# Performance work log

Measured on AMD Instinct MI355X. Metric: run time of the kernel, lower is better.

The kernel has to match this reference:

```python
import jax, jax.numpy as jnp
import numpy as np


def setup_inputs() -> dict:
    key = jax.random.key(0)
    k1, k2 = jax.random.split(key)
    S_src, S_tgt, B, H = 2048, 2048, 16, 256
    out_e = jax.random.normal(k1, (S_src, B, 2 * H), dtype=jnp.float32)
    out_d = jax.random.normal(k2, (S_tgt, B, H), dtype=jnp.float32)
    return {"out_e": out_e, "out_d": out_d}


def reference(out_e, out_d):
    # out_e: [S_src, B, 2*H] (bidirectional), out_d: [S_tgt, B, H]
    S, B, H2 = out_e.shape
    # sum the two directions: [S, B, H]
    enc = out_e.reshape(S, B, 2, H2 // 2).sum(axis=2)
    enc = enc.transpose(1, 0, 2)   # [B, S_src, H]
    dec = out_d.transpose(1, 0, 2)  # [B, S_tgt, H]
    # attn scores [B, S_src, S_tgt]; softmax over source positions (dim=1)
    attn = jnp.einsum('bsh,bth->bst', enc, dec)
    attn = jax.nn.softmax(attn, axis=1)
    # context: weighted sum over source positions -> [B, S_tgt, H]
    context = jnp.einsum('bst,bsh->bth', attn, enc)
    return context.transpose(1, 0, 2)  # [S_tgt, B, H]
```

## Files before the change

### kernel.cpp

```cpp
#include <hip/hip_runtime.h>
#include <stdint.h>
#include <stddef.h>

#define BATCH 16
#define SEQ 2048
#define HDIM 256
#define SCHUNK 32
#define TTILE 128
#define NCHUNK 64
#define TILE_U16 8192
#define NTILES 1024
#define KSTRIDE 260
#define PSTRIDE 40

typedef float f32x4 __attribute__((ext_vector_type(4)));
typedef float f32x16 __attribute__((ext_vector_type(16)));
typedef _Float16 f16x8 __attribute__((ext_vector_type(8)));
typedef __bf16 bf16x8 __attribute__((ext_vector_type(8)));
typedef unsigned short u16;
typedef u16 u16x4 __attribute__((ext_vector_type(4)));
typedef u16 u16x8 __attribute__((ext_vector_type(8)));
typedef unsigned int u32;
typedef const __attribute__((address_space(1))) u32* gp1_t;
typedef __attribute__((address_space(3))) u32* lp3_t;

static __device__ __forceinline__ u16 f2bf(float f) {
  union { float f; unsigned int u; } v; v.f = f;
  unsigned int u = v.u;
  unsigned int r = u + 0x7FFFu + ((u >> 16) & 1u);
  return (u16)(r >> 16);
}

__global__ __launch_bounds__(256, 4)
void prepass_kernel(const float* __restrict__ e,
                    u16* __restrict__ KH, u16* __restrict__ VT) {
  __shared__ float Ks[SCHUNK * KSTRIDE];
  const int tid = threadIdx.x;
  const int b  = blockIdx.x >> 6;
  const int ck = blockIdx.x & 63;
  const size_t tile = (size_t)blockIdx.x * TILE_U16;

  {
    int row = tid >> 3;
    int c8  = tid & 7;
    const float* src = e + ((size_t)(ck * SCHUNK + row) * BATCH + b) * (2 * HDIM);
#pragma unroll
    for (int u = 0; u < 8; ++u) {
      int col = c8 * 4 + 32 * u;
      float4 xa = *(const float4*)(src + col);
      float4 xb = *(const float4*)(src + col + HDIM);
      float4 s; s.x = xa.x + xb.x; s.y = xa.y + xb.y; s.z = xa.z + xb.z; s.w = xa.w + xb.w;
      *(float4*)&Ks[row * KSTRIDE + col] = s;
    }
  }
  __syncthreads();

  const int lane = tid & 63;
  const int w = tid >> 6;
  const int m = lane & 31;
  const int g = lane >> 5;

#pragma unroll
  for (int i = 0; i < 4; ++i) {
    int kb = w * 4 + i;
    const float* rp = &Ks[m * KSTRIDE + kb * 16 + g * 8];
    u16x8 hi;
#pragma unroll
    for (int j = 0; j < 8; ++j)
      hi[j] = __builtin_bit_cast(u16, (_Float16)rp[j]);
    *(u16x8*)&KH[tile + (size_t)(kb * 64 + lane) * 8] = hi;
  }

#pragma unroll
  for (int i = 0; i < 4; ++i) {
    int fr = w * 4 + i;
    int ht = fr >> 1, ka = fr & 1;
    u16x8 v;
#pragma unroll
    for (int j = 0; j < 8; ++j)
      v[j] = f2bf(Ks[(ka * 16 + g * 8 + j) * KSTRIDE + ht * 32 + m]);
    *(u16x8*)&VT[tile + (size_t)(fr * 64 + lane) * 8] = v;
  }
}

__global__ __launch_bounds__(512, 2)
void attn_main_kernel(const u16* __restrict__ KH, const u16* __restrict__ VT,
                      const float* __restrict__ dq,
                      float* __restrict__ out) {
  __shared__ alignas(16) u16 KHs[4][TILE_U16];
  __shared__ alignas(16) u16 VTs[4][TILE_U16];
  __shared__ alignas(16) u16 Pb[8][32 * PSTRIDE];

  const int tid  = threadIdx.x;
  const int lane = tid & 63;
  const int wv   = tid >> 6;
  const int wq   = wv & 3;
  const int grp  = wv >> 2;
  const int m    = lane & 31;
  const int g    = lane >> 5;

  const int b  = blockIdx.x >> 4;
  const int t0 = (blockIdx.x & 15) * TTILE;

  const int tq = t0 + wq * 32 + m;
  const float* qp = dq + ((size_t)tq * BATCH + b) * HDIM;
  f16x8 qh[16];
#pragma unroll
  for (int kb = 0; kb < 16; ++kb) {
    int h = kb * 16 + g * 8;
    float4 f0 = *(const float4*)(qp + h);
    float4 f1 = *(const float4*)(qp + h + 4);
    float xs[8] = {f0.x, f0.y, f0.z, f0.w, f1.x, f1.y, f1.z, f1.w};
    u16x8 hb;
#pragma unroll
    for (int j = 0; j < 8; ++j)
      hb[j] = __builtin_bit_cast(u16, (_Float16)xs[j]);
    qh[kb] = __builtin_bit_cast(f16x8, hb);
  }

  f32x16 ctx[8];
#pragma unroll
  for (int ht = 0; ht < 8; ++ht) ctx[ht] = (f32x16)(0.0f);
  float dsum = 0.0f;

  const bool isVT  = (wv >> 1) & 1;
  const int  choff = wv >> 2;
  const int  subbase = (wv & 1) * 8;
  const u16* srcArr = isVT ? VT : KH;
  auto stage = [&](int jpair) {
    int ckk = 2 * jpair + choff;
    int buf = ckk & 3;
    size_t tb = ((size_t)b * NCHUNK + ckk) * TILE_U16;
    u16* dst = isVT ? &VTs[buf][0] : &KHs[buf][0];
#pragma unroll
    for (int i = 0; i < 8; ++i) {
      int sub = subbase + i;
      __builtin_amdgcn_global_load_lds(
          (gp1_t)(const void*)&srcArr[tb + (size_t)sub * 512 + lane * 8],
          (lp3_t)(void*)&dst[sub * 512], 16, 0, 0);
    }
  };

  stage(0);

  for (int j = 0; j < 32; ++j) {
    __syncthreads();
    if (j < 31) stage(j + 1);
    const int ckk = 2 * j + grp;
    const int buf = ckk & 3;

    f32x16 a0 = (f32x16)(0.0f), a1 = (f32x16)(0.0f);
#pragma unroll
    for (int kb = 0; kb < 16; kb += 2) {
      f16x8 k0 = __builtin_bit_cast(f16x8, *(const u16x8*)&KHs[buf][kb * 512 + lane * 8]);
      f16x8 k1 = __builtin_bit_cast(f16x8, *(const u16x8*)&KHs[buf][(kb + 1) * 512 + lane * 8]);
      a0 = __builtin_amdgcn_mfma_f32_32x32x16_f16(k0, qh[kb], a0, 0, 0, 0);
      a1 = __builtin_amdgcn_mfma_f32_32x32x16_f16(k1, qh[kb + 1], a1, 0, 0, 0);
    }

    u16 pbits[16];
#pragma unroll
    for (int r = 0; r < 16; ++r) {
      float pf = __expf(a0[r] + a1[r] - 128.0f);
      dsum += pf;
      pbits[r] = f2bf(pf);
    }
#pragma unroll
    for (int rr = 0; rr < 4; ++rr) {
      u16x4 w4 = {pbits[4 * rr], pbits[4 * rr + 1], pbits[4 * rr + 2], pbits[4 * rr + 3]};
      *(u16x4*)&Pb[wv][m * PSTRIDE + rr * 8 + g * 4] = w4;
    }
    bf16x8 pa0 = __builtin_bit_cast(bf16x8, *(const u16x8*)&Pb[wv][m * PSTRIDE + g * 8]);
    bf16x8 pa1 = __builtin_bit_cast(bf16x8, *(const u16x8*)&Pb[wv][m * PSTRIDE + 16 + g * 8]);

#pragma unroll
    for (int ht = 0; ht < 8; ++ht) {
      bf16x8 v0 = __builtin_bit_cast(bf16x8, *(const u16x8*)&VTs[buf][(ht * 2) * 512 + lane * 8]);
      bf16x8 v1 = __builtin_bit_cast(bf16x8, *(const u16x8*)&VTs[buf][(ht * 2 + 1) * 512 + lane * 8]);
      ctx[ht] = __builtin_amdgcn_mfma_f32_32x32x16_bf16(pa0, v0, ctx[ht], 0, 0, 0);
      ctx[ht] = __builtin_amdgcn_mfma_f32_32x32x16_bf16(pa1, v1, ctx[ht], 0, 0, 0);
    }
  }

  dsum += __shfl_xor(dsum, 32, 64);
  __syncthreads();

  float* exch = (wq < 2) ? (float*)&KHs[wq * 2][0] : (float*)&VTs[(wq - 2) * 2][0];

  if (grp == 1) {
#pragma unroll
    for (int r4 = 0; r4 < 4; ++r4)
#pragma unroll
      for (int ht = 0; ht < 8; ++ht) {
        f32x4 v = {ctx[ht][r4 * 4], ctx[ht][r4 * 4 + 1],
                   ctx[ht][r4 * 4 + 2], ctx[ht][r4 * 4 + 3]};
        *(f32x4*)&exch[r4 * 2048 + ht * 256 + lane * 4] = v;
      }
    ((float*)&Pb[wv][0])[lane] = dsum;
  }
  __syncthreads();

  if (grp == 0) {
    float dB = ((const float*)&Pb[wv + 4][0])[lane];
    float inv = 1.0f / (dsum + dB);
#pragma unroll
    for (int r4 = 0; r4 < 4; ++r4)
#pragma unroll
      for (int ht = 0; ht < 8; ++ht) {
        f32x4 v = *(const f32x4*)&exch[r4 * 2048 + ht * 256 + lane * 4];
        ctx[ht][r4 * 4]     += v[0];
        ctx[ht][r4 * 4 + 1] += v[1];
        ctx[ht][r4 * 4 + 2] += v[2];
        ctx[ht][r4 * 4 + 3] += v[3];
      }
#pragma unroll
    for (int r = 0; r < 16; ++r) {
      int tl = (r & 3) + 8 * (r >> 2) + 4 * g;
      float rinv = __shfl(inv, tl, 64);
      int t = t0 + wq * 32 + tl;
      float* op = out + ((size_t)t * BATCH + b) * HDIM + m;
#pragma unroll
      for (int ht = 0; ht < 8; ++ht)
        op[ht * 32] = ctx[ht][r] * rinv;
    }
  }
}

extern "C" void kernel_launch(void* const* d_in, const int* in_sizes, int n_in,
                              void* d_out, int out_size, void* d_ws, size_t ws_size,
                              hipStream_t stream) {
  const float* e  = (const float*)d_in[0];
  const float* dq = (const float*)d_in[1];
  float* out = (float*)d_out;
  u16* KH = (u16*)d_ws;
  u16* VT = KH + (size_t)NTILES * TILE_U16;
  prepass_kernel<<<dim3(NTILES), dim3(256), 0, stream>>>(e, KH, VT);
  attn_main_kernel<<<dim3(BATCH * (SEQ / TTILE)), dim3(512), 0, stream>>>(
      KH, VT, dq, out);
}
```

Measured before the change: 204.6 us.

## Software-pipeline QK and PV stages across chunk pairs in attention main loop

Restructures the main loop so each iteration computes the QK scores for the current chunk pair while doing the PV MFMA for the previous pair, using the exp'd probabilities from the last iteration. K tiles are prefetched one pair ahead and V tiles are loaded a pair later, with a prologue and epilogue to fill and drain the pipeline. The interleaving lets the two kinds of MFMA overlap with the exp/conversion work, at the cost of more live registers (two extra accumulators and the carried P fragments). The exp reduction is also split into two partial sums.

New measurement: 524.9 us. 157% more time.

```diff
diff --git a/kernel.cpp b/kernel.cpp
--- a/kernel.cpp
+++ b/kernel.cpp
@@ -8,6 +8,7 @@
 #define SCHUNK 32
 #define TTILE 128
 #define NCHUNK 64
+#define NPAIR 32
 #define TILE_U16 8192
 #define NTILES 1024
 #define KSTRIDE 260
@@ -122,63 +123,129 @@
 #pragma unroll
   for (int ht = 0; ht < 8; ++ht) ctx[ht] = (f32x16)(0.0f);
   float dsum = 0.0f;
-
-  const bool isVT  = (wv >> 1) & 1;
-  const int  choff = wv >> 2;
-  const int  subbase = (wv & 1) * 8;
-  const u16* srcArr = isVT ? VT : KH;
-  auto stage = [&](int jpair) {
-    int ckk = 2 * jpair + choff;
-    int buf = ckk & 3;
-    size_t tb = ((size_t)b * NCHUNK + ckk) * TILE_U16;
-    u16* dst = isVT ? &VTs[buf][0] : &KHs[buf][0];
-#pragma unroll
-    for (int i = 0; i < 8; ++i) {
-      int sub = subbase + i;
+  f32x16 accA, accB;
+  bf16x8 pa0, pa1;
+
+  const size_t bbase = (size_t)b * NCHUNK;
+
+  {
+    int c = wv >> 2;
+    int sb4 = (wv & 3) * 4;
+    size_t tb = (bbase + c) * TILE_U16;
+    u16* dst = &KHs[c][0];
+#pragma unroll
+    for (int i = 0; i < 4; ++i) {
+      int sub = sb4 + i;
       __builtin_amdgcn_global_load_lds(
-          (gp1_t)(const void*)&srcArr[tb + (size_t)sub * 512 + lane * 8],
+          (gp1_t)(const void*)&KH[tb + (size_t)sub * 512 + lane * 8],
           (lp3_t)(void*)&dst[sub * 512], 16, 0, 0);
     }
+  }
+
+  const int role = wv >> 1;
+  const int par  = role & 1;
+  const int sb   = (wv & 1) * 8;
+
+  auto stage_iter = [&](int j) {
+    if (role < 2) {
+      int pair = j + 1;
+      if (pair < NPAIR) {
+        int c = 2 * pair + par;
+        size_t tb = (bbase + c) * TILE_U16;
+        u16* dst = &KHs[c & 3][0];
+#pragma unroll
+        for (int i = 0; i < 8; ++i) {
+          int sub = sb + i;
+          __builtin_amdgcn_global_load_lds(
+              (gp1_t)(const void*)&KH[tb + (size_t)sub * 512 + lane * 8],
+              (lp3_t)(void*)&dst[sub * 512], 16, 0, 0);
+        }
+      }
+    } else {
+      int c = 2 * j + par;
+      size_t tb = (bbase + c) * TILE_U16;
+      u16* dst = &VTs[c & 3][0];
+#pragma unroll
+      for (int i = 0; i < 8; ++i) {
+        int sub = sb + i;
+        __builtin_amdgcn_global_load_lds(
+            (gp1_t)(const void*)&VT[tb + (size_t)sub * 512 + lane * 8],
+            (lp3_t)(void*)&dst[sub * 512], 16, 0, 0);
+      }
+    }
   };
 
-  stage(0);
-
-  for (int j = 0; j < 32; ++j) {
-    __syncthreads();
-    if (j < 31) stage(j + 1);
-    const int ckk = 2 * j + grp;
-    const int buf = ckk & 3;
-
-    f32x16 a0 = (f32x16)(0.0f), a1 = (f32x16)(0.0f);
-#pragma unroll
-    for (int kb = 0; kb < 16; kb += 2) {
-      f16x8 k0 = __builtin_bit_cast(f16x8, *(const u16x8*)&KHs[buf][kb * 512 + lane * 8]);
-      f16x8 k1 = __builtin_bit_cast(f16x8, *(const u16x8*)&KHs[buf][(kb + 1) * 512 + lane * 8]);
-      a0 = __builtin_amdgcn_mfma_f32_32x32x16_f16(k0, qh[kb], a0, 0, 0, 0);
-      a1 = __builtin_amdgcn_mfma_f32_32x32x16_f16(k1, qh[kb + 1], a1, 0, 0, 0);
-    }
-
+  auto expP = [&]() {
     u16 pbits[16];
-#pragma unroll
-    for (int r = 0; r < 16; ++r) {
-      float pf = __expf(a0[r] + a1[r] - 128.0f);
-      dsum += pf;
-      pbits[r] = f2bf(pf);
-    }
+    float l0 = 0.f, l1 = 0.f;
+#pragma unroll
+    for (int r = 0; r < 16; r += 2) {
+      float pf0 = __expf(accA[r] + accB[r] - 128.0f);
+      float pf1 = __expf(accA[r + 1] + accB[r + 1] - 128.0f);
+      l0 += pf0; l1 += pf1;
+      pbits[r] = f2bf(pf0); pbits[r + 1] = f2bf(pf1);
+    }
+    dsum += l0 + l1;
 #pragma unroll
     for (int rr = 0; rr < 4; ++rr) {
       u16x4 w4 = {pbits[4 * rr], pbits[4 * rr + 1], pbits[4 * rr + 2], pbits[4 * rr + 3]};
       *(u16x4*)&Pb[wv][m * PSTRIDE + rr * 8 + g * 4] = w4;
     }
-    bf16x8 pa0 = __builtin_bit_cast(bf16x8, *(const u16x8*)&Pb[wv][m * PSTRIDE + g * 8]);
-    bf16x8 pa1 = __builtin_bit_cast(bf16x8, *(const u16x8*)&Pb[wv][m * PSTRIDE + 16 + g * 8]);
-
-#pragma unroll
-    for (int ht = 0; ht < 8; ++ht) {
-      bf16x8 v0 = __builtin_bit_cast(bf16x8, *(const u16x8*)&VTs[buf][(ht * 2) * 512 + lane * 8]);
-      bf16x8 v1 = __builtin_bit_cast(bf16x8, *(const u16x8*)&VTs[buf][(ht * 2 + 1) * 512 + lane * 8]);
-      ctx[ht] = __builtin_amdgcn_mfma_f32_32x32x16_bf16(pa0, v0, ctx[ht], 0, 0, 0);
-      ctx[ht] = __builtin_amdgcn_mfma_f32_32x32x16_bf16(pa1, v1, ctx[ht], 0, 0, 0);
+    pa0 = __builtin_bit_cast(bf16x8, *(const u16x8*)&Pb[wv][m * PSTRIDE + g * 8]);
+    pa1 = __builtin_bit_cast(bf16x8, *(const u16x8*)&Pb[wv][m * PSTRIDE + 16 + g * 8]);
+  };
+
+  __syncthreads();
+  stage_iter(0);
+  {
+    const u16* KHb = &KHs[grp][0];
+    f32x16 nA = (f32x16)(0.0f), nB = (f32x16)(0.0f);
+#pragma unroll
+    for (int i = 0; i < 8; ++i) {
+      f16x8 k0 = __builtin_bit_cast(f16x8, *(const u16x8*)&KHb[(2 * i) * 512 + lane * 8]);
+      f16x8 k1 = __builtin_bit_cast(f16x8, *(const u16x8*)&KHb[(2 * i + 1) * 512 + lane * 8]);
+      nA = __builtin_amdgcn_mfma_f32_32x32x16_f16(k0, qh[2 * i], nA, 0, 0, 0);
+      nB = __builtin_amdgcn_mfma_f32_32x32x16_f16(k1, qh[2 * i + 1], nB, 0, 0, 0);
+    }
+    accA = nA; accB = nB;
+  }
+
+#pragma unroll 2
+  for (int j = 1; j < NPAIR; ++j) {
+    __syncthreads();
+    stage_iter(j);
+    expP();
+
+    const int ck_q = 2 * j + grp;
+    const int ck_v = ck_q - 2;
+    const u16* KHb = &KHs[ck_q & 3][0];
+    const u16* VTb = &VTs[ck_v & 3][0];
+    f32x16 nA = (f32x16)(0.0f), nB = (f32x16)(0.0f);
+#pragma unroll
+    for (int i = 0; i < 8; ++i) {
+      f16x8 k0 = __builtin_bit_cast(f16x8, *(const u16x8*)&KHb[(2 * i) * 512 + lane * 8]);
+      f16x8 k1 = __builtin_bit_cast(f16x8, *(const u16x8*)&KHb[(2 * i + 1) * 512 + lane * 8]);
+      bf16x8 v0 = __builtin_bit_cast(bf16x8, *(const u16x8*)&VTb[(2 * i) * 512 + lane * 8]);
+      bf16x8 v1 = __builtin_bit_cast(bf16x8, *(const u16x8*)&VTb[(2 * i + 1) * 512 + lane * 8]);
+      nA = __builtin_amdgcn_mfma_f32_32x32x16_f16(k0, qh[2 * i], nA, 0, 0, 0);
+      ctx[i] = __builtin_amdgcn_mfma_f32_32x32x16_bf16(pa0, v0, ctx[i], 0, 0, 0);
+      nB = __builtin_amdgcn_mfma_f32_32x32x16_f16(k1, qh[2 * i + 1], nB, 0, 0, 0);
+      ctx[i] = __builtin_amdgcn_mfma_f32_32x32x16_bf16(pa1, v1, ctx[i], 0, 0, 0);
+    }
+    accA = nA; accB = nB;
+  }
+
+  __syncthreads();
+  expP();
+  {
+    const int ck_v = 2 * (NPAIR - 1) + grp;
+    const u16* VTb = &VTs[ck_v & 3][0];
+#pragma unroll
+    for (int i = 0; i < 8; ++i) {
+      bf16x8 v0 = __builtin_bit_cast(bf16x8, *(const u16x8*)&VTb[(2 * i) * 512 + lane * 8]);
+      bf16x8 v1 = __builtin_bit_cast(bf16x8, *(const u16x8*)&VTb[(2 * i + 1) * 512 + lane * 8]);
+      ctx[i] = __builtin_amdgcn_mfma_f32_32x32x16_bf16(pa0, v0, ctx[i], 0, 0, 0);
+      ctx[i] = __builtin_amdgcn_mfma_f32_32x32x16_bf16(pa1, v1, ctx[i], 0, 0, 0);
     }
   }
 
```
